# Performance work log

Measured on AMD Instinct MI355X. Metric: run time of the kernel, lower is better.

## Reference

```python
import jax, jax.numpy as jnp
import numpy as np

NUM_HEADS = 8
HEAD_SPLITS = [2, 3, 3]   # heads per conv window group (windows 3,5,7)


def _dwconv(x, w, b):
    # depthwise conv2d, SAME padding; x [B,Cg,H,W], w [Cg,1,k,k]
    k = w.shape[-1]
    pad = k // 2
    out = jax.lax.conv_general_dilated(
        x, w, window_strides=(1, 1), padding=[(pad, pad), (pad, pad)],
        feature_group_count=x.shape[1])
    return out + b[None, :, None, None]


def setup_inputs() -> dict:
    key = jax.random.key(0)
    ks = jax.random.split(key, 8)
    B, Hs, Ws, C = 16, 56, 56, 512
    N = 1 + Hs * Ws
    Ch = C // NUM_HEADS
    inp = {
        "x": jax.random.normal(ks[0], (B, N, C), dtype=jnp.float32),
        "qkv_w": jax.random.normal(ks[1], (3 * C, C), dtype=jnp.float32) * 0.02,
        "qkv_b": jnp.zeros((3 * C,), dtype=jnp.float32),
        "proj_w": jax.random.normal(ks[2], (C, C), dtype=jnp.float32) * 0.02,
        "proj_b": jnp.zeros((C,), dtype=jnp.float32),
        "conv_w3": jax.random.normal(ks[3], (2 * Ch, 1, 3, 3), dtype=jnp.float32) * 0.1,
        "conv_b3": jnp.zeros((2 * Ch,), dtype=jnp.float32),
        "conv_w5": jax.random.normal(ks[4], (3 * Ch, 1, 5, 5), dtype=jnp.float32) * 0.1,
        "conv_b5": jnp.zeros((3 * Ch,), dtype=jnp.float32),
        "conv_w7": jax.random.normal(ks[5], (3 * Ch, 1, 7, 7), dtype=jnp.float32) * 0.1,
        "conv_b7": jnp.zeros((3 * Ch,), dtype=jnp.float32),
        "H": 56,
        "W": 56,
    }
    return inp


def reference(x, qkv_w, qkv_b, proj_w, proj_b,
              conv_w3, conv_b3, conv_w5, conv_b5, conv_w7, conv_b7, H, W):
    B, N, C = x.shape
    h = NUM_HEADS
    Ch = C // h
    scale = Ch ** -0.5

    # qkv projection -> [3, B, h, N, Ch]
    qkv = (x @ qkv_w.T + qkv_b).reshape(B, N, 3, h, Ch)
    qkv = jnp.transpose(qkv, (2, 0, 3, 1, 4))
    q, k, v = qkv[0], qkv[1], qkv[2]

    # linear-attention factorization: softmax over tokens, then small Ch x Ch matmuls
    k_sm = jax.nn.softmax(k, axis=2)                     # softmax over N
    kv = jnp.einsum('bhnk,bhnd->bhkd', k_sm, v)          # [B,h,Ch,Ch]
    factor_att = jnp.einsum('bhnk,bhkd->bhnd', q, kv)    # [B,h,N,Ch]

    # conv relative-position encoding (CoaT ConvRelPosEnc)
    q_img = q[:, :, 1:, :]                               # drop CLS token
    v_img = v[:, :, 1:, :]
    v_img = jnp.transpose(v_img, (0, 1, 3, 2)).reshape(B, h * Ch, H, W)
    splits = np.cumsum([s * Ch for s in HEAD_SPLITS])[:-1]
    p3, p5, p7 = jnp.split(v_img, splits, axis=1)
    conv_v = jnp.concatenate([
        _dwconv(p3, conv_w3, conv_b3),
        _dwconv(p5, conv_w5, conv_b5),
        _dwconv(p7, conv_w7, conv_b7)], axis=1)           # [B,h*Ch,H,W]
    conv_v = jnp.transpose(conv_v.reshape(B, h, Ch, H * W), (0, 1, 3, 2))
    ev = q_img * conv_v                                   # [B,h,HW,Ch]
    crpe = jnp.concatenate(
        [jnp.zeros((B, h, 1, Ch), dtype=x.dtype), ev], axis=2)

    out = scale * factor_att + crpe                       # [B,h,N,Ch]
    out = jnp.transpose(out, (0, 2, 1, 3)).reshape(B, N, C)
    return out @ proj_w.T + proj_b
```

## Files before the change

### kernel.cpp

```cpp
#include <hip/hip_runtime.h>
#include <stdint.h>

#define NHEADS 8
#define NTOK   3137
#define BATCH  16
#define CDIM   512
#define MT     (BATCH*NTOK)

typedef unsigned short u16;
typedef float f32x4  __attribute__((ext_vector_type(4)));
typedef short bf16x8 __attribute__((ext_vector_type(8)));

__device__ __forceinline__ float bf2f(u16 u){
  union { uint32_t i; float f; } x; x.i = ((uint32_t)u) << 16; return x.f;
}
__device__ __forceinline__ u16 f2bf(float f){
  union { float f; uint32_t i; } x; x.f = f;
  uint32_t r = x.i + 0x7fffu + ((x.i >> 16) & 1u);
  return (u16)(r >> 16);
}
__device__ __forceinline__ void async_ld16(void* lds, const void* g){
  __builtin_amdgcn_global_load_lds((const __attribute__((address_space(1))) void*)g,
                                   (__attribute__((address_space(3))) void*)lds, 16, 0, 0);
}
#define MFMA16(d,a,b) d = __builtin_amdgcn_mfma_f32_16x16x32_bf16(a,b,d,0,0,0)

__global__ void cvt_kernel(const float* __restrict__ src, u16* __restrict__ dst, int n4){
  int i = blockIdx.x * blockDim.x + threadIdx.x;
  if (i < n4){
    float4 v = ((const float4*)src)[i];
    uint32_t lo = ((uint32_t)f2bf(v.y) << 16) | f2bf(v.x);
    uint32_t hi = ((uint32_t)f2bf(v.w) << 16) | f2bf(v.z);
    ((uint2*)dst)[i] = make_uint2(lo, hi);
  }
}

template<int MODE>
__global__ __launch_bounds__(512, 2) void gemm2(
    const u16* __restrict__ A, const u16* __restrict__ Bw, const float* __restrict__ bias,
    u16* __restrict__ q_s, u16* __restrict__ k_s, u16* __restrict__ v_s,
    float* __restrict__ outF, int M)
{
  constexpr int BM=256, BN=256, WN=4;
  constexpr int THREADS = 512;
  constexpr int MF = 8, NF = 4;
  constexpr int WROWS = 128, WCOLS = 64;
  __shared__ __align__(16) u16 smem[2*(BM+BN)*64];

  const int t = threadIdx.x;
  const int w = t >> 6, l = t & 63;
  const int wr = w / WN, wc = w % WN;
  const int lr = l & 15, lg = l >> 4;

  const int nx = gridDim.x;
  const int nwg = nx * gridDim.y;
  const int orig = blockIdx.y * nx + blockIdx.x;
  const int q8 = nwg >> 3, r8 = nwg & 7;
  const int xcd = orig & 7;
  const int wgid = (xcd < r8 ? xcd*(q8+1) : r8*(q8+1) + (xcd-r8)*q8) + (orig >> 3);
  const int n0 = (wgid % nx) * BN;
  const int m0 = (wgid / nx) * BM;

  f32x4 acc[MF][NF];
#pragma unroll
  for (int i=0;i<MF;i++)
#pragma unroll
    for (int j=0;j<NF;j++) acc[i][j] = (f32x4){0.f,0.f,0.f,0.f};

  auto stage = [&](int bi, int k0){
    u16* da = smem + bi*(BM*64);
    u16* db = smem + 2*BM*64 + bi*(BN*64);
#pragma unroll
    for (int j=0;j<(BM*8)/THREADS;j++){
      int qc = t + THREADS*j;
      int R = qc >> 3, c = qc & 7;
      int cs = (c ^ (R & 7)) * 8;
      int ar = m0 + R; if (ar > M-1) ar = M-1;
      async_ld16(&da[qc*8], &A[(size_t)ar*512 + k0 + cs]);
    }
#pragma unroll
    for (int j=0;j<(BN*8)/THREADS;j++){
      int qc = t + THREADS*j;
      int R = qc >> 3, c = qc & 7;
      int cs = (c ^ (R & 7)) * 8;
      async_ld16(&db[qc*8], &Bw[(size_t)(n0+R)*512 + k0 + cs]);
    }
  };

  stage(0, 0);
  __syncthreads();
  int cur = 0;
  for (int kt = 0; kt < 8; ++kt){
    if (kt < 7) stage(cur ^ 1, (kt+1)*64);
    const u16* a_base = smem + cur*(BM*64);
    const u16* b_base = smem + 2*BM*64 + cur*(BN*64);
    __builtin_amdgcn_s_setprio(1);
#pragma unroll
    for (int ks=0; ks<2; ks++){
      bf16x8 af[MF], bfv[NF];
      int chunk = ks*4 + lg;
#pragma unroll
      for (int fi=0;fi<MF;fi++){
        int row = wr*WROWS + fi*16 + lr;
        af[fi] = *(const bf16x8*)&a_base[row*64 + ((chunk ^ (row & 7))*8)];
      }
#pragma unroll
      for (int fj=0;fj<NF;fj++){
        int col = wc*WCOLS + fj*16 + lr;
        bfv[fj] = *(const bf16x8*)&b_base[col*64 + ((chunk ^ (col & 7))*8)];
      }
#pragma unroll
      for (int fi=0;fi<MF;fi++)
#pragma unroll
        for (int fj=0;fj<NF;fj++)
          acc[fi][fj] = __builtin_amdgcn_mfma_f32_16x16x32_bf16(af[fi], bfv[fj], acc[fi][fj], 0, 0, 0);
    }
    __builtin_amdgcn_s_setprio(0);
    __syncthreads();
    cur ^= 1;
  }

  float bvv[NF];
#pragma unroll
  for (int fj=0;fj<NF;fj++) bvv[fj] = bias[n0 + wc*WCOLS + fj*16 + lr];

  if (MODE == 0){
    u16* warea = smem + w * (WROWS*WCOLS);
#pragma unroll
    for (int fi=0;fi<MF;fi++)
#pragma unroll
      for (int fj=0;fj<NF;fj++)
#pragma unroll
        for (int r=0;r<4;r++)
          warea[(fi*16 + lg*4 + r)*WCOLS + fj*16 + lr] = f2bf(acc[fi][fj][r] + bvv[fj]);
    __syncthreads();
    const int colo = n0 + wc*WCOLS;
    const int part = colo >> 9;
    const int hq   = (colo >> 6) & 7;
    u16* dst = (part == 0) ? q_s : ((part == 1) ? k_s : v_s);
    const int rsub = l >> 3;
    const int csub = (l & 7) * 8;
#pragma unroll
    for (int pass=0; pass<WROWS/8; ++pass){
      int rl = pass*8 + rsub;
      int m = m0 + wr*WROWS + rl;
      if (m < M){
        int bb = m / NTOK;
        int n  = m - bb*NTOK;
        uint4 vv = *(const uint4*)&warea[rl*WCOLS + csub];
        *(uint4*)&dst[((size_t)(bb*8 + hq)*NTOK + n)*64 + csub] = vv;
      }
    }
  } else {
    constexpr int PR = WROWS/2;
    float* warea = (float*)smem + w * (PR*WCOLS);
    const int colo = n0 + wc*WCOLS;
    const int rsub = l >> 4;
    const int csub = (l & 15) * 4;
#pragma unroll
    for (int p=0; p<2; ++p){
#pragma unroll
      for (int fh=0; fh<MF/2; fh++){
        int fi = p*(MF/2) + fh;
#pragma unroll
        for (int fj=0;fj<NF;fj++)
#pragma unroll
          for (int r=0;r<4;r++)
            warea[(fh*16 + lg*4 + r)*WCOLS + fj*16 + lr] = acc[fi][fj][r] + bvv[fj];
      }
#pragma unroll
      for (int pass=0; pass<PR/4; ++pass){
        int rl = pass*4 + rsub;
        int m = m0 + wr*WROWS + p*PR + rl;
        if (m < M){
          float4 vv = *(const float4*)&warea[rl*WCOLS + csub];
          *(float4*)&outF[(size_t)m*512 + colo + csub] = vv;
        }
      }
    }
  }
}

__global__ __launch_bounds__(256) void kv_mfma(
    const u16* __restrict__ k_s, const u16* __restrict__ v_s,
    float* __restrict__ kv_p, float* __restrict__ s_p)
{
  __shared__ __align__(16) u16 ekT[64*64];
  __shared__ __align__(16) u16 vT[64*64];
  __shared__ float part_s[32*64];
  const int t  = threadIdx.x;
  const int bh = blockIdx.x;
  const int qq = blockIdx.y;
  const size_t base = (size_t)bh * NTOK * 64;
  const int c_beg = qq*6 + (qq < 2 ? qq : 2);
  const int c_end = c_beg + 6 + (qq < 2 ? 1 : 0);
  const int w = t >> 6, l = t & 63;
  const int lr = l & 15, lg = l >> 4;
  const int nl0 = t >> 3;
  const int dc  = (t & 7) * 8;

  f32x4 acc[4];
#pragma unroll
  for (int j=0;j<4;j++) acc[j] = (f32x4){0.f,0.f,0.f,0.f};
  float s_loc[8];
#pragma unroll
  for (int i=0;i<8;i++) s_loc[i] = 0.f;

  auto LD = [&](int ch, int half, uint4& kv, uint4& vv){
    int n = ch*64 + nl0 + half*32;
    if (n < NTOK){
      kv = *(const uint4*)&k_s[base + (size_t)n*64 + dc];
      vv = *(const uint4*)&v_s[base + (size_t)n*64 + dc];
    } else {
      kv = make_uint4(0u,0u,0u,0u);
      vv = make_uint4(0u,0u,0u,0u);
    }
  };

  uint4 kc0, vc0, kc1, vc1, kn0, vn0, kn1, vn1;
  LD(c_beg, 0, kc0, vc0);
  LD(c_beg, 1, kc1, vc1);

  for (int ch = c_beg; ch < c_end; ++ch){
    const int n0c = ch*64;
    if (ch + 1 < c_end){ LD(ch+1, 0, kn0, vn0); LD(ch+1, 1, kn1, vn1); }
    __syncthreads();
#pragma unroll
    for (int half=0; half<2; ++half){
      const uint4& kvec = half ? kc1 : kc0;
      const uint4& vvec = half ? vc1 : vc0;
      int nloc = nl0 + half*32;
      bool valid = (n0c + nloc < NTOK);
      const u16* kp = (const u16*)&kvec;
      const u16* vp = (const u16*)&vvec;
      const int nc = nloc >> 3, ne = nloc & 7;
#pragma unroll
      for (int i=0;i<8;i++){
        float e = valid ? __expf(bf2f(kp[i])) : 0.f;
        s_loc[i] += e;
        int row = dc + i;
        int pos = row*64 + ((nc ^ (row & 7) ^ ((row >> 3) & 7))*8) + ne;
        ekT[pos] = f2bf(e);
        vT[pos]  = vp[i];
      }
    }
    __syncthreads();
    __builtin_amdgcn_s_setprio(1);
#pragma unroll
    for (int ks=0; ks<2; ks++){
      int chnk = ks*4 + lg;
      int arow = w*16 + lr;
      bf16x8 af = *(const bf16x8*)&ekT[arow*64 + ((chnk ^ (arow & 7) ^ ((arow >> 3) & 7))*8)];
#pragma unroll
      for (int fj=0; fj<4; fj++){
        int col = fj*16 + lr;
        bf16x8 bv = *(const bf16x8*)&vT[col*64 + ((chnk ^ (col & 7) ^ ((col >> 3) & 7))*8)];
        MFMA16(acc[fj], af, bv);
      }
    }
    __builtin_amdgcn_s_setprio(0);
    kc0 = kn0; vc0 = vn0; kc1 = kn1; vc1 = vn1;
  }

  const size_t obase = ((size_t)qq*128 + bh) * 4096;
#pragma unroll
  for (int fj=0; fj<4; fj++)
#pragma unroll
    for (int r=0; r<4; r++)
      kv_p[obase + (size_t)(w*16 + lg*4 + r)*64 + fj*16 + lr] = acc[fj][r];

#pragma unroll
  for (int i=0;i<8;i++) part_s[nl0*64 + dc + i] = s_loc[i];
  __syncthreads();
  if (t < 64){
    float s = 0.f;
    for (int r=0;r<32;r++) s += part_s[r*64 + t];
    s_p[((size_t)qq*128 + bh)*64 + t] = s;
  }
}

__global__ void kv_reduce(const float* __restrict__ kv_p, const float* __restrict__ s_p,
                          const u16* __restrict__ q_s, u16* __restrict__ kvT,
                          u16* __restrict__ out_pre){
  __shared__ float red[64*64];
  const int bh = blockIdx.x, t = threadIdx.x;
  const int b = bh >> 3, h = bh & 7;
  const int k = t >> 2;
  const float q0 = bf2f(q_s[(size_t)bh*NTOK*64 + k]);
  float S = 0.f;
#pragma unroll
  for (int hf=0; hf<8; hf++) S += s_p[(hf*128 + bh)*64 + k];
  const float rS = 1.f / S;
  for (int i=0;i<16;i++){
    int e = t*16 + i;
    int d = (t & 3)*16 + i;
    float v = 0.f;
#pragma unroll
    for (int hf=0; hf<8; hf++) v += kv_p[(size_t)(hf*128 + bh)*4096 + e];
    float val = v * rS;
    kvT[(size_t)bh*4096 + d*64 + k] = f2bf(val);
    red[k*64 + d] = val * q0;
  }
  __syncthreads();
  if (t < 64){
    float s = 0.f;
    for (int r=0;r<64;r++) s += red[r*64 + t];
    out_pre[((size_t)b*NTOK)*CDIM + h*64 + t] = f2bf(0.125f * s);
  }
}

template<int R>
__global__ __launch_bounds__(256) void conv_fa(
    const u16* __restrict__ v_s, const u16* __restrict__ q_s,
    const u16* __restrict__ kvT,
    const float* __restrict__ wsrc, const float* __restrict__ bsrc,
    int h0, u16* __restrict__ out_pre)
{
  constexpr int KK = 2*R + 1;
  constexpr int TAPS = KK*KK;
  __shared__ __align__(16) u16 smem[8192 + KK*3584];
  u16* vt = smem + 8192;
  const int t = threadIdx.x;
  const int y  = blockIdx.x;
  const int hh = blockIdx.y;
  const int b  = blockIdx.z;
  const int h  = h0 + hh;
  const int bh = b*8 + h;
  const size_t base = (size_t)bh * NTOK * 64;
  const int n0 = 1 + y*56;

#pragma unroll
  for (int j=0;j<2;j++){
    int qq = t + 256*j;
    int row = qq >> 3, c = qq & 7;
    int cs = (c ^ (row & 7)) * 8;
    int n = n0 + row; if (n > NTOK-1) n = NTOK-1;
    async_ld16(&smem[qq*8], &q_s[base + (size_t)n*64 + cs]);
    async_ld16(&smem[4096 + qq*8], &kvT[(size_t)bh*4096 + row*64 + cs]);
  }
  for (int ry=0; ry<KK; ry++){
    int yy = y - R + ry;
    for (int idx = t; idx < 448; idx += 256){
      uint4 val = make_uint4(0u,0u,0u,0u);
      if (yy >= 0 && yy < 56)
        val = *(const uint4*)&v_s[base + (size_t)(1 + yy*56)*64 + idx*8];
      *(uint4*)&vt[ry*3584 + idx*8] = val;
    }
  }
  __syncthreads();

  const int w = t >> 6, l = t & 63;
  const int lr = l & 15, lg = l >> 4;
  f32x4 fac[4];
#pragma unroll
  for (int j=0;j<4;j++) fac[j] = (f32x4){0.f,0.f,0.f,0.f};
#pragma unroll
  for (int ks=0; ks<2; ks++){
    int chunk = ks*4 + lg;
    int arow = w*16 + lr;
    bf16x8 af = *(const bf16x8*)&smem[arow*64 + ((chunk ^ (arow & 7))*8)];
#pragma unroll
    for (int fj=0; fj<4; fj++){
      int col = fj*16 + lr;
      bf16x8 bvv = *(const bf16x8*)&smem[4096 + col*64 + ((chunk ^ (col & 7))*8)];
      MFMA16(fac[fj], af, bvv);
    }
  }

  const int d = l;
  const int xg = w;
  float wreg[TAPS];
#pragma unroll
  for (int i=0;i<TAPS;i++) wreg[i] = wsrc[(hh*64 + d)*TAPS + i];
  const float bias = bsrc[hh*64 + d];
  float creg[14];
#pragma unroll
  for (int i=0;i<14;i++) creg[i] = bias;
  const int x0 = xg * 14;
#pragma unroll
  for (int ry=0; ry<KK; ry++){
    float rw[14 + 2*R];
#pragma unroll
    for (int i=0; i<14+2*R; i++){
      int xx = x0 - R + i;
      rw[i] = (xx >= 0 && xx < 56) ? bf2f(vt[ry*3584 + xx*64 + d]) : 0.f;
    }
#pragma unroll
    for (int xi=0; xi<14; xi++)
#pragma unroll
      for (int rx=0; rx<KK; rx++)
        creg[xi] += rw[xi+rx] * wreg[ry*KK + rx];
  }

  float qv[14];
#pragma unroll
  for (int xi=0; xi<14; xi++){
    int row = x0 + xi;
    int chunk = d >> 3, e = d & 7;
    qv[xi] = bf2f(smem[row*64 + ((chunk ^ (row & 7))*8) + e]);
  }

  __syncthreads();
  float* fa = (float*)smem;
#pragma unroll
  for (int fj=0; fj<4; fj++)
#pragma unroll
    for (int r=0; r<4; r++)
      fa[(w*16 + lg*4 + r)*64 + fj*16 + lr] = 0.125f * fac[fj][r];
  __syncthreads();

#pragma unroll
  for (int xi=0; xi<14; xi++){
    int nn = n0 + x0 + xi;
    out_pre[((size_t)b*NTOK + nn)*CDIM + h*64 + d] =
        f2bf(fa[(x0 + xi)*64 + d] + creg[xi]*qv[xi]);
  }
}

extern "C" void kernel_launch(void* const* d_in, const int* in_sizes, int n_in,
                              void* d_out, int out_size, void* d_ws, size_t ws_size,
                              hipStream_t stream)
{
  const float* x      = (const float*)d_in[0];
  const float* qkv_w  = (const float*)d_in[1];
  const float* qkv_b  = (const float*)d_in[2];
  const float* proj_w = (const float*)d_in[3];
  const float* proj_b = (const float*)d_in[4];
  const float* w3 = (const float*)d_in[5];
  const float* b3 = (const float*)d_in[6];
  const float* w5 = (const float*)d_in[7];
  const float* b5 = (const float*)d_in[8];
  const float* w7 = (const float*)d_in[9];
  const float* b7 = (const float*)d_in[10];
  float* out = (float*)d_out;

  char* ws = (char*)d_ws;
  size_t off = 0;
  auto alloc = [&](size_t bytes) -> void* {
    void* p = ws + off;
    off += (bytes + 255) & ~(size_t)255;
    return p;
  };
  u16*   x_bf     = (u16*)alloc((size_t)MT*512*2);
  u16*   qkvw_bf  = (u16*)alloc((size_t)1536*512*2);
  u16*   projw_bf = (u16*)alloc((size_t)512*512*2);
  u16*   q_s      = (u16*)alloc((size_t)128*NTOK*64*2);
  u16*   k_s      = (u16*)alloc((size_t)128*NTOK*64*2);
  u16*   v_s      = (u16*)alloc((size_t)128*NTOK*64*2);
  u16*   kvT      = (u16*)alloc((size_t)128*4096*2);
  float* kv_p     = (float*)alloc((size_t)8*128*4096*4);
  float* s_p      = (float*)alloc((size_t)8*128*64*4);
  u16*   out_pre  = x_bf;

  { int n4 = (MT*512)/4;   cvt_kernel<<<(n4+255)/256, 256, 0, stream>>>(x, x_bf, n4); }
  { int n4 = (1536*512)/4; cvt_kernel<<<(n4+255)/256, 256, 0, stream>>>(qkv_w, qkvw_bf, n4); }
  { int n4 = (512*512)/4;  cvt_kernel<<<(n4+255)/256, 256, 0, stream>>>(proj_w, projw_bf, n4); }

  gemm2<0><<<dim3(6, 197), 512, 0, stream>>>(x_bf, qkvw_bf, qkv_b, q_s, k_s, v_s, nullptr, MT);

  kv_mfma<<<dim3(128, 8), 256, 0, stream>>>(k_s, v_s, kv_p, s_p);
  kv_reduce<<<128, 256, 0, stream>>>(kv_p, s_p, q_s, kvT, out_pre);

  conv_fa<1><<<dim3(56, 2, 16), 256, 0, stream>>>(v_s, q_s, kvT, w3, b3, 0, out_pre);
  conv_fa<2><<<dim3(56, 3, 16), 256, 0, stream>>>(v_s, q_s, kvT, w5, b5, 2, out_pre);
  conv_fa<3><<<dim3(56, 3, 16), 256, 0, stream>>>(v_s, q_s, kvT, w7, b7, 5, out_pre);

  gemm2<1><<<dim3(2, 197), 512, 0, stream>>>(out_pre, projw_bf, proj_b, nullptr, nullptr, nullptr, out, MT);
}
```

Measured before the change: 345.9 us.

## Shrink GEMM tiles to 128x128 single-buffered and merge conversion kernels

Replaces the 256x256 double-buffered 512-thread GEMM with a 128x128 single-buffered 256-thread version that uses explicit vmcnt waits and raw barriers, which cuts shared memory per block so more blocks can be resident. It also fuses the three fp32-to-bf16 conversion launches into one kernel. The smaller tiles give less operand reuse per block, and without double buffering the loads no longer overlap with MFMA work inside a block. Overlap now has to come from running more blocks at once.

```diff
diff --git a/kernel.cpp b/kernel.cpp
--- a/kernel.cpp
+++ b/kernel.cpp
@@ -23,33 +23,36 @@
   __builtin_amdgcn_global_load_lds((const __attribute__((address_space(1))) void*)g,
                                    (__attribute__((address_space(3))) void*)lds, 16, 0, 0);
 }
+#define BARM()   asm volatile("s_barrier" ::: "memory")
+#define WAITV(N) asm volatile("s_waitcnt vmcnt(" #N ")" ::: "memory")
 #define MFMA16(d,a,b) d = __builtin_amdgcn_mfma_f32_16x16x32_bf16(a,b,d,0,0,0)
 
-__global__ void cvt_kernel(const float* __restrict__ src, u16* __restrict__ dst, int n4){
+__global__ void cvt_all(const float* __restrict__ x, u16* __restrict__ x_bf,
+                        const float* __restrict__ qw, u16* __restrict__ qw_bf,
+                        const float* __restrict__ pw, u16* __restrict__ pw_bf){
+  const int n4x = (MT*512)/4, n4q = (1536*512)/4, n4p = (512*512)/4;
   int i = blockIdx.x * blockDim.x + threadIdx.x;
-  if (i < n4){
-    float4 v = ((const float4*)src)[i];
-    uint32_t lo = ((uint32_t)f2bf(v.y) << 16) | f2bf(v.x);
-    uint32_t hi = ((uint32_t)f2bf(v.w) << 16) | f2bf(v.z);
-    ((uint2*)dst)[i] = make_uint2(lo, hi);
-  }
+  const float* src; u16* dst; int j = i;
+  if (i < n4x){ src = x; dst = x_bf; }
+  else if (i < n4x + n4q){ src = qw; dst = qw_bf; j = i - n4x; }
+  else if (i < n4x + n4q + n4p){ src = pw; dst = pw_bf; j = i - n4x - n4q; }
+  else return;
+  float4 v = ((const float4*)src)[j];
+  uint32_t lo = ((uint32_t)f2bf(v.y) << 16) | f2bf(v.x);
+  uint32_t hi = ((uint32_t)f2bf(v.w) << 16) | f2bf(v.z);
+  ((uint2*)dst)[j] = make_uint2(lo, hi);
 }
 
 template<int MODE>
-__global__ __launch_bounds__(512, 2) void gemm2(
+__global__ __launch_bounds__(256) void gemmM(
     const u16* __restrict__ A, const u16* __restrict__ Bw, const float* __restrict__ bias,
     u16* __restrict__ q_s, u16* __restrict__ k_s, u16* __restrict__ v_s,
     float* __restrict__ outF, int M)
 {
-  constexpr int BM=256, BN=256, WN=4;
-  constexpr int THREADS = 512;
-  constexpr int MF = 8, NF = 4;
-  constexpr int WROWS = 128, WCOLS = 64;
-  __shared__ __align__(16) u16 smem[2*(BM+BN)*64];
-
+  __shared__ __align__(16) u16 smem[256*64];
   const int t = threadIdx.x;
   const int w = t >> 6, l = t & 63;
-  const int wr = w / WN, wc = w % WN;
+  const int wr = w >> 1, wc = w & 1;
   const int lr = l & 15, lg = l >> 4;
 
   const int nx = gridDim.x;
@@ -58,122 +61,113 @@
   const int q8 = nwg >> 3, r8 = nwg & 7;
   const int xcd = orig & 7;
   const int wgid = (xcd < r8 ? xcd*(q8+1) : r8*(q8+1) + (xcd-r8)*q8) + (orig >> 3);
-  const int n0 = (wgid % nx) * BN;
-  const int m0 = (wgid / nx) * BM;
-
-  f32x4 acc[MF][NF];
-#pragma unroll
-  for (int i=0;i<MF;i++)
-#pragma unroll
-    for (int j=0;j<NF;j++) acc[i][j] = (f32x4){0.f,0.f,0.f,0.f};
-
-  auto stage = [&](int bi, int k0){
-    u16* da = smem + bi*(BM*64);
-    u16* db = smem + 2*BM*64 + bi*(BN*64);
-#pragma unroll
-    for (int j=0;j<(BM*8)/THREADS;j++){
-      int qc = t + THREADS*j;
+  const int n0 = (wgid % nx) * 128;
+  const int m0 = (wgid / nx) * 128;
+
+  f32x4 acc[4][4];
+#pragma unroll
+  for (int i=0;i<4;i++)
+#pragma unroll
+    for (int j=0;j<4;j++) acc[i][j] = (f32x4){0.f,0.f,0.f,0.f};
+
+  u16* da = smem;
+  u16* db = smem + 128*64;
+
+  for (int kt = 0; kt < 8; ++kt){
+    const int k0 = kt*64;
+#pragma unroll
+    for (int j=0;j<4;j++){
+      int qc = t + 256*j;
       int R = qc >> 3, c = qc & 7;
       int cs = (c ^ (R & 7)) * 8;
       int ar = m0 + R; if (ar > M-1) ar = M-1;
       async_ld16(&da[qc*8], &A[(size_t)ar*512 + k0 + cs]);
     }
 #pragma unroll
-    for (int j=0;j<(BN*8)/THREADS;j++){
-      int qc = t + THREADS*j;
+    for (int j=0;j<4;j++){
+      int qc = t + 256*j;
       int R = qc >> 3, c = qc & 7;
       int cs = (c ^ (R & 7)) * 8;
       async_ld16(&db[qc*8], &Bw[(size_t)(n0+R)*512 + k0 + cs]);
     }
-  };
-
-  stage(0, 0);
-  __syncthreads();
-  int cur = 0;
-  for (int kt = 0; kt < 8; ++kt){
-    if (kt < 7) stage(cur ^ 1, (kt+1)*64);
-    const u16* a_base = smem + cur*(BM*64);
-    const u16* b_base = smem + 2*BM*64 + cur*(BN*64);
+    WAITV(0);
+    BARM();
     __builtin_amdgcn_s_setprio(1);
 #pragma unroll
     for (int ks=0; ks<2; ks++){
-      bf16x8 af[MF], bfv[NF];
+      bf16x8 af[4], bfv[4];
       int chunk = ks*4 + lg;
 #pragma unroll
-      for (int fi=0;fi<MF;fi++){
-        int row = wr*WROWS + fi*16 + lr;
-        af[fi] = *(const bf16x8*)&a_base[row*64 + ((chunk ^ (row & 7))*8)];
-      }
-#pragma unroll
-      for (int fj=0;fj<NF;fj++){
-        int col = wc*WCOLS + fj*16 + lr;
-        bfv[fj] = *(const bf16x8*)&b_base[col*64 + ((chunk ^ (col & 7))*8)];
-      }
-#pragma unroll
-      for (int fi=0;fi<MF;fi++)
-#pragma unroll
-        for (int fj=0;fj<NF;fj++)
+      for (int fi=0;fi<4;fi++){
+        int row = wr*64 + fi*16 + lr;
+        af[fi] = *(const bf16x8*)&da[row*64 + ((chunk ^ (row & 7))*8)];
+      }
+#pragma unroll
+      for (int fj=0;fj<4;fj++){
+        int col = wc*64 + fj*16 + lr;
+        bfv[fj] = *(const bf16x8*)&db[col*64 + ((chunk ^ (col & 7))*8)];
+      }
+#pragma unroll
+      for (int fi=0;fi<4;fi++)
+#pragma unroll
+        for (int fj=0;fj<4;fj++)
           acc[fi][fj] = __builtin_amdgcn_mfma_f32_16x16x32_bf16(af[fi], bfv[fj], acc[fi][fj], 0, 0, 0);
     }
     __builtin_amdgcn_s_setprio(0);
-    __syncthreads();
-    cur ^= 1;
-  }
-
-  float bvv[NF];
-#pragma unroll
-  for (int fj=0;fj<NF;fj++) bvv[fj] = bias[n0 + wc*WCOLS + fj*16 + lr];
+    BARM();
+  }
+
+  float bvv[4];
+#pragma unroll
+  for (int fj=0;fj<4;fj++) bvv[fj] = bias[n0 + wc*64 + fj*16 + lr];
+  const int colo = n0 + wc*64;
 
   if (MODE == 0){
-    u16* warea = smem + w * (WROWS*WCOLS);
-#pragma unroll
-    for (int fi=0;fi<MF;fi++)
-#pragma unroll
-      for (int fj=0;fj<NF;fj++)
+    u16* warea = smem + w * 4096;
+#pragma unroll
+    for (int fi=0;fi<4;fi++)
+#pragma unroll
+      for (int fj=0;fj<4;fj++)
 #pragma unroll
         for (int r=0;r<4;r++)
-          warea[(fi*16 + lg*4 + r)*WCOLS + fj*16 + lr] = f2bf(acc[fi][fj][r] + bvv[fj]);
-    __syncthreads();
-    const int colo = n0 + wc*WCOLS;
+          warea[(fi*16 + lg*4 + r)*64 + fj*16 + lr] = f2bf(acc[fi][fj][r] + bvv[fj]);
     const int part = colo >> 9;
     const int hq   = (colo >> 6) & 7;
     u16* dst = (part == 0) ? q_s : ((part == 1) ? k_s : v_s);
     const int rsub = l >> 3;
     const int csub = (l & 7) * 8;
 #pragma unroll
-    for (int pass=0; pass<WROWS/8; ++pass){
+    for (int pass=0; pass<8; ++pass){
       int rl = pass*8 + rsub;
-      int m = m0 + wr*WROWS + rl;
+      int m = m0 + wr*64 + rl;
       if (m < M){
         int bb = m / NTOK;
         int n  = m - bb*NTOK;
-        uint4 vv = *(const uint4*)&warea[rl*WCOLS + csub];
+        uint4 vv = *(const uint4*)&warea[rl*64 + csub];
         *(uint4*)&dst[((size_t)(bb*8 + hq)*NTOK + n)*64 + csub] = vv;
       }
     }
   } else {
-    constexpr int PR = WROWS/2;
-    float* warea = (float*)smem + w * (PR*WCOLS);
-    const int colo = n0 + wc*WCOLS;
+    float* warea = (float*)smem + w * 2048;
     const int rsub = l >> 4;
     const int csub = (l & 15) * 4;
 #pragma unroll
     for (int p=0; p<2; ++p){
 #pragma unroll
-      for (int fh=0; fh<MF/2; fh++){
-        int fi = p*(MF/2) + fh;
-#pragma unroll
-        for (int fj=0;fj<NF;fj++)
+      for (int fh=0; fh<2; fh++){
+        int fi = p*2 + fh;
+#pragma unroll
+        for (int fj=0;fj<4;fj++)
 #pragma unroll
           for (int r=0;r<4;r++)
-            warea[(fh*16 + lg*4 + r)*WCOLS + fj*16 + lr] = acc[fi][fj][r] + bvv[fj];
-      }
-#pragma unroll
-      for (int pass=0; pass<PR/4; ++pass){
+            warea[(fh*16 + lg*4 + r)*64 + fj*16 + lr] = acc[fi][fj][r] + bvv[fj];
+      }
+#pragma unroll
+      for (int pass=0; pass<8; ++pass){
         int rl = pass*4 + rsub;
-        int m = m0 + wr*WROWS + p*PR + rl;
+        int m = m0 + wr*64 + p*32 + rl;
         if (m < M){
-          float4 vv = *(const float4*)&warea[rl*WCOLS + csub];
+          float4 vv = *(const float4*)&warea[rl*64 + csub];
           *(float4*)&outF[(size_t)m*512 + colo + csub] = vv;
         }
       }
@@ -452,11 +446,10 @@
   float* s_p      = (float*)alloc((size_t)8*128*64*4);
   u16*   out_pre  = x_bf;
 
-  { int n4 = (MT*512)/4;   cvt_kernel<<<(n4+255)/256, 256, 0, stream>>>(x, x_bf, n4); }
-  { int n4 = (1536*512)/4; cvt_kernel<<<(n4+255)/256, 256, 0, stream>>>(qkv_w, qkvw_bf, n4); }
-  { int n4 = (512*512)/4;  cvt_kernel<<<(n4+255)/256, 256, 0, stream>>>(proj_w, projw_bf, n4); }
-
-  gemm2<0><<<dim3(6, 197), 512, 0, stream>>>(x_bf, qkvw_bf, qkv_b, q_s, k_s, v_s, nullptr, MT);
+  { int n4 = (MT*512 + 1536*512 + 512*512)/4;
+    cvt_all<<<(n4+255)/256, 256, 0, stream>>>(x, x_bf, qkv_w, qkvw_bf, proj_w, projw_bf); }
+
+  gemmM<0><<<dim3(12, 393), 256, 0, stream>>>(x_bf, qkvw_bf, qkv_b, q_s, k_s, v_s, nullptr, MT);
 
   kv_mfma<<<dim3(128, 8), 256, 0, stream>>>(k_s, v_s, kv_p, s_p);
   kv_reduce<<<128, 256, 0, stream>>>(kv_p, s_p, q_s, kvT, out_pre);
@@ -465,5 +458,5 @@
   conv_fa<2><<<dim3(56, 3, 16), 256, 0, stream>>>(v_s, q_s, kvT, w5, b5, 2, out_pre);
   conv_fa<3><<<dim3(56, 3, 16), 256, 0, stream>>>(v_s, q_s, kvT, w7, b7, 5, out_pre);
 
-  gemm2<1><<<dim3(2, 197), 512, 0, stream>>>(out_pre, projw_bf, proj_b, nullptr, nullptr, nullptr, out, MT);
-}
+  gemmM<1><<<dim3(4, 393), 256, 0, stream>>>(out_pre, projw_bf, proj_b, nullptr, nullptr, nullptr, out, MT);
+}
```

Result: no change. 342.4 us (-1.0%).
